# Kernel tuning notes

Hardware: AMD Instinct MI355X
Metric: run time of the kernel (lower is better)

## Reference

```python
import jax, jax.numpy as jnp
import numpy as np

B = 65536
DIM = 8
HIS_LEN = 5
KIND_LEN = 10
HIS_ITEM_DIM = (1 + KIND_LEN) * DIM  # 88
ALL_DIM = DIM * (5 + KIND_LEN) + HIS_ITEM_DIM  # 208


def _linear_params(key, in_dim, out_dim):
    k1, k2 = jax.random.split(key)
    bound = 1.0 / np.sqrt(in_dim)
    w = jax.random.uniform(k1, (out_dim, in_dim), jnp.float32, -bound, bound)
    b = jax.random.uniform(k2, (out_dim,), jnp.float32, -bound, bound)
    return w, b


def setup_inputs() -> dict:
    key = jax.random.key(0)
    ks = jax.random.split(key, 20)
    inp = {
        'userid': jax.random.randint(ks[0], (B, 1), 0, 1000000),
        'itemid': jax.random.randint(ks[1], (B, 1), 0, 1000000),
        'user_age': jax.random.randint(ks[2], (B, 1), 0, 8),
        'gender': jax.random.randint(ks[3], (B, 1), 0, 3),
        'user_occupation': jax.random.randint(ks[4], (B, 1), 0, 25),
        'item_kind': jax.random.randint(ks[5], (B, KIND_LEN), 0, 20),
        'item_id_his': jax.random.randint(ks[6], (B, HIS_LEN), 0, 1000000),
        'item_kind_his': jax.random.randint(ks[7], (B, HIS_LEN, KIND_LEN), 0, 20),
        'user_emb': jax.random.normal(ks[8], (1000000, DIM), jnp.float32),
        'item_emb': jax.random.normal(ks[9], (1000000, DIM), jnp.float32),
        'age_emb': jax.random.normal(ks[10], (8, DIM), jnp.float32),
        'gender_emb': jax.random.normal(ks[11], (3, DIM), jnp.float32),
        'occ_emb': jax.random.normal(ks[12], (25, DIM), jnp.float32),
        'kind_emb': jax.random.normal(ks[13], (20, DIM), jnp.float32),
    }
    act_dims = [(HIS_ITEM_DIM * 3, 64), (64, 32), (32, 1)]
    for i, (di, do) in enumerate(act_dims, 1):
        w, b = _linear_params(jax.random.fold_in(key, 100 + i), di, do)
        inp[f'act_w{i}'], inp[f'act_b{i}'] = w, b
    mlp_dims = [(ALL_DIM, 128), (128, 64), (64, 32), (32, 1)]
    for i, (di, do) in enumerate(mlp_dims, 1):
        w, b = _linear_params(jax.random.fold_in(key, 200 + i), di, do)
        inp[f'mlp_w{i}'], inp[f'mlp_b{i}'] = w, b
    return inp


def _forward(userid, itemid, user_age, gender, user_occupation, item_kind,
             item_id_his, item_kind_his, user_emb, item_emb, age_emb,
             gender_emb, occ_emb, kind_emb,
             act_w1, act_b1, act_w2, act_b2, act_w3, act_b3,
             mlp_w1, mlp_b1, mlp_w2, mlp_b2, mlp_w3, mlp_b3, mlp_w4, mlp_b4):
    b = userid.shape[0]
    user_w = user_emb[userid]          # [b,1,8]
    item_w = item_emb[itemid]          # [b,1,8]
    age_w = age_emb[user_age]          # [b,1,8]
    gen_w = gender_emb[gender]         # [b,1,8]
    occ_w = occ_emb[user_occupation]   # [b,1,8]
    kind_w = kind_emb[item_kind]       # [b,10,8]
    kind_w = kind_w * (item_kind != 0)[..., None].astype(kind_w.dtype)

    # history: vectorized over his_len
    his_item_w = item_emb[item_id_his]           # [b,5,8]
    his_kind_w = kind_emb[item_kind_his]         # [b,5,10,8]
    his_kind_w = his_kind_w * (item_kind_his != 0)[..., None].astype(his_kind_w.dtype)
    his_feature = jnp.concatenate([his_item_w[:, :, None, :], his_kind_w], axis=2)
    his_feature = his_feature.reshape(b, HIS_LEN, HIS_ITEM_DIM)  # [b,5,88]

    item_feat_now = jnp.concatenate([item_w, kind_w], axis=1).reshape(b, 1, HIS_ITEM_DIM)
    item_feat_now = jnp.broadcast_to(item_feat_now, (b, HIS_LEN, HIS_ITEM_DIM))

    # ActUnit: i_in = [i1, i1-i2, i2]; score = MLP(i_in); act_weight = i1 * score
    i1, i2 = his_feature, item_feat_now
    i_in = jnp.concatenate([i1, i1 - i2, i2], axis=-1)  # [b,5,264]
    h = jax.nn.relu(jnp.einsum('bsd,od->bso', i_in, act_w1) + act_b1)
    h = jax.nn.relu(jnp.einsum('bsd,od->bso', h, act_w2) + act_b2)
    score = jnp.einsum('bsd,od->bso', h, act_w3) + act_b3  # [b,5,1]
    act_weight = i1 * score
    his_pool = jnp.sum(his_feature * act_weight, axis=1)  # [b,88]

    all_feat = jnp.concatenate([user_w, item_w, age_w, gen_w, occ_w, kind_w], axis=1).reshape(b, -1)
    all_feat = jnp.concatenate([all_feat, his_pool], axis=-1)  # [b,208]

    h = jax.nn.relu(all_feat @ mlp_w1.T + mlp_b1)
    h = jax.nn.relu(h @ mlp_w2.T + mlp_b2)
    h = jax.nn.relu(h @ mlp_w3.T + mlp_b3)
    logit = h @ mlp_w4.T + mlp_b4  # [b,1]
    return jax.nn.sigmoid(logit)


def reference(userid, itemid, user_age, gender, user_occupation, item_kind,
              item_id_his, item_kind_his, user_emb, item_emb, age_emb,
              gender_emb, occ_emb, kind_emb,
              act_w1, act_b1, act_w2, act_b2, act_w3, act_b3,
              mlp_w1, mlp_b1, mlp_w2, mlp_b2, mlp_w3, mlp_b3, mlp_w4, mlp_b4):
    return _forward(userid, itemid, user_age, gender, user_occupation, item_kind,
                    item_id_his, item_kind_his, user_emb, item_emb, age_emb,
                    gender_emb, occ_emb, kind_emb,
                    act_w1, act_b1, act_w2, act_b2, act_w3, act_b3,
                    mlp_w1, mlp_b1, mlp_w2, mlp_b2, mlp_w3, mlp_b3, mlp_w4, mlp_b4)
```

## Files before the change

kernel.cpp:

```cpp
#include <hip/hip_runtime.h>
#include <cstdint>
#include <math.h>

#define BATCH    65536
#define HIS_LEN  5
#define KIND_LEN 10
#define SB       64
#define NTH      256

typedef float    v2f __attribute__((ext_vector_type(2)));
typedef float    v4f __attribute__((ext_vector_type(4)));
typedef _Float16 v2h __attribute__((ext_vector_type(2)));
typedef _Float16 v8h __attribute__((ext_vector_type(8)));
__device__ __forceinline__ v2f mk2(float a, float b){ v2f r; r.x=a; r.y=b; return r; }
#define C2H(u)  __builtin_bit_cast(v2h,(unsigned)(u))
#define C8H(u4) __builtin_bit_cast(v8h,(u4))

#if __has_builtin(__builtin_amdgcn_fdot2)
__device__ __forceinline__ float FD2(v2h a, v2h b, float c){
  return __builtin_amdgcn_fdot2(a, b, c, false);
}
#else
__device__ __forceinline__ float FD2(v2h a, v2h b, float c){
  return c + (float)a.x*(float)b.x + (float)a.y*(float)b.y;
}
#endif

__device__ __forceinline__ unsigned short f2h(float f){
  return __builtin_bit_cast(unsigned short, (_Float16)f);
}
__device__ __forceinline__ unsigned pack2h(float a, float b){
  return (unsigned)f2h(a) | ((unsigned)f2h(b) << 16);
}
__device__ __forceinline__ v2h pkh(float a, float b){
  return __builtin_bit_cast(v2h, __builtin_amdgcn_cvt_pkrtz(a, b));
}

#define OFF_HW1F 0
#define OFF_AW2F 6144
#define OFF_PF   7168
#define OFF_M3H  7428
#define OFF_MW1F 8452
#define OFF_MB1  22788
#define OFF_MW2F 22916
#define PREP_N   27012
#define AW2F4 1536
#define M3H4  1857
#define MW1F4 2113
#define MW2F4 5729

#define X2B   0
#define X1B   832
#define H1B   1664
#define H2B   2240
#define M3HL  2816
#define LAB1  12312
#define LAB2  12376
#define LW3   12408
#define LAB3  12440
#define LMB2  12441
#define LMB3  12505
#define LM4   12537
#define LMB4  12569
#define MB1F  12572
#define LDSF  12700

typedef const float* fp;

__device__ __forceinline__ float m1s_val(fp m1, int o, int q, int t){
  if(t >= 52) return 0.f;
  int src;
  if(t<8){ int E = (q==0)?0:(8+8*q); src = E + t; }
  else if(t<30){ int d=t-8; int idx = 8*(d>>1)+2*q+(d&1);
                 src = (idx<8) ? (8+idx) : (32+idx); }
  else { int d=t-30; int idx = 8*(d>>1)+2*q+(d&1); src = 120+idx; }
  return m1[o*208 + src];
}
__device__ __forceinline__ float m1k(fp m1, int o, int k){
  return m1s_val(m1, o, k/56, k%56);
}
__device__ __forceinline__ float w1c_val(fp aw1, int o, int q, int h, int d){
  if(d >= 22) return 0.f;
  int idx = 8*(d>>1) + 2*q + (d&1);
  return h ? (aw1[o*264+176+idx] - aw1[o*264+88+idx])
           : (aw1[o*264+idx]     + aw1[o*264+88+idx]);
}
__device__ __forceinline__ float hw1v(fp aw1, int o, int k){
  int h = (k >= 96) ? 1 : 0;
  int kk = k - 96*h;
  int q = kk/24, d = kk%24;
  return (d<22) ? w1c_val(aw1,o,q,h,d) : 0.f;
}

__global__ void din_prep(fp aw1, fp ab1, fp aw2, fp ab2, fp aw3, fp ab3,
                         fp m1,  fp mb1, fp m2,  fp mb2, fp m3,  fp mb3,
                         fp m4,  fp mb4, float* __restrict__ ws){
  int j = blockIdx.x*blockDim.x + threadIdx.x;
  unsigned* wsu = (unsigned*)ws;
  if(j < 6144){
    int frag = j>>2, jr = j&3;
    int lane = frag & 63, nt = frag >> 6;
    int n = nt/6, t = nt%6;
    int o = 16*n + (lane&15);
    int k0 = t*32 + ((lane>>4)<<3) + 2*jr;
    wsu[OFF_HW1F + j] = pack2h(hw1v(aw1,o,k0), hw1v(aw1,o,k0+1));
    return;
  } j -= 6144;
  if(j < 1024){
    int frag = j>>2, jr = j&3;
    int lane = frag & 63, nt = frag >> 6;
    int n2 = nt>>1, t2 = nt&1;
    int o = 16*n2 + (lane&15);
    int k0 = t2*32 + ((lane>>4)<<3) + 2*jr;
    wsu[OFF_AW2F + j] = pack2h(aw2[o*64 + k0], aw2[o*64 + k0+1]);
    return;
  } j -= 1024;
  if(j < 258){
    float v;
    if(j < 64)       v = ab1[j];
    else if(j < 96)  v = ab2[j-64];
    else if(j < 128) v = aw3[j-96];
    else if(j < 129) v = ab3[0];
    else if(j < 193) v = mb2[j-129];
    else if(j < 225) v = mb3[j-193];
    else if(j < 257) v = m4[j-225];
    else             v = mb4[0];
    ws[OFF_PF + j] = v; return;
  } j -= 258;
  if(j < 2){ ws[OFF_PF+258+j] = 0.f; return; } j -= 2;
  if(j < 1024){
    int qq = j>>8, rr = j&255, ip = rr>>5, dw = rr&31;
    wsu[OFF_M3H + j] = pack2h(m3[dw*64 + 16*qq + 2*ip], m3[dw*64 + 16*qq + 2*ip+1]);
    return;
  } j -= 1024;
  if(j < 14336){
    int frag = j>>2, jr = j&3;
    int lane = frag & 63, nt = frag >> 6;
    int n = nt/7, t = nt - 7*n;
    int o = 16*n + (lane&15);
    int k0 = t*32 + ((lane>>4)<<3) + 2*jr;
    wsu[OFF_MW1F + j] = pack2h(m1k(m1,o,k0), m1k(m1,o,k0+1));
    return;
  } j -= 14336;
  if(j < 128){ ws[OFF_MB1 + j] = mb1[j]; return; } j -= 128;
  if(j < 4096){
    int frag = j>>2, jr = j&3;
    int lane = frag & 63, nt = frag >> 6;
    int n2 = nt>>2, t2 = nt&3;
    int o = 16*n2 + (lane&15);
    int k0 = t2*32 + ((lane>>4)<<3) + 2*jr;
    wsu[OFF_MW2F + j] = pack2h(m2[o*128 + k0], m2[o*128 + k0+1]);
    return;
  }
}

template<int CTL>
__device__ __forceinline__ float qp(float v){
  return __uint_as_float((unsigned)__builtin_amdgcn_update_dpp(
      0, (int)__float_as_uint(v), CTL, 0xF, 0xF, true));
}
__device__ __forceinline__ float bsum4(float v){
  v += qp<0xB1>(v);
  v += qp<0x4E>(v);
  return v;
}

__device__ __forceinline__ void ldst16(void* l, const void* g){
  __builtin_amdgcn_global_load_lds(
      (const __attribute__((address_space(1))) unsigned int*)(uintptr_t)g,
      (__attribute__((address_space(3))) unsigned int*)(uintptr_t)l, 16, 0, 0);
}
__device__ __forceinline__ void ldst4(void* l, const void* g){
  __builtin_amdgcn_global_load_lds(
      (const __attribute__((address_space(1))) unsigned int*)(uintptr_t)g,
      (__attribute__((address_space(3))) unsigned int*)(uintptr_t)l, 4, 0, 0);
}

__device__ __forceinline__ void gather_h(const float2* __restrict__ itemp,
                                         const float2* __restrict__ kindp,
                                         int item_idx, const int* __restrict__ kidx,
                                         int q, v2h* f){
  float2 v = itemp[item_idx*4 + q];
  f[0] = pkh(v.x, v.y);
  #pragma unroll
  for(int r=0;r<KIND_LEN;r++){
    int ki = kidx[r];
    float2 w = kindp[ki*4 + q];
    float mx = ki ? w.x : 0.f, my = ki ? w.y : 0.f;
    f[1+r] = pkh(mx, my);
  }
}

__device__ __forceinline__ void write_X(float4* ls4, int base, int wid, int q,
                                        const v2h* f){
  unsigned xd[12];
  #pragma unroll
  for(int r=0;r<11;r++) xd[r] = __builtin_bit_cast(unsigned, f[r]);
  xd[11] = 0;
  uint4* xp = (uint4*)(ls4 + base + wid*13 + 3*q);
  #pragma unroll
  for(int c=0;c<3;c++){
    uint4 t; t.x=xd[4*c]; t.y=xd[4*c+1]; t.z=xd[4*c+2]; t.w=xd[4*c+3];
    xp[c] = t;
  }
}

__global__ void __launch_bounds__(NTH, 3)
din_main(const int* __restrict__ userid, const int* __restrict__ itemid,
         const int* __restrict__ age,    const int* __restrict__ gen,
         const int* __restrict__ occ,    const int* __restrict__ item_kind,
         const int* __restrict__ his_id, const int* __restrict__ his_kind,
         const float2* __restrict__ user_emb, const float2* __restrict__ item_emb,
         const float2* __restrict__ age_emb,  const float2* __restrict__ gen_emb,
         const float2* __restrict__ occ_emb,  const float2* __restrict__ kind_emb,
         const float* __restrict__ ws, float* __restrict__ out){
  const int tid  = threadIdx.x;
  const int q    = tid & 3;
  const int sl   = (tid & 63) >> 2;
  const int wv   = __builtin_amdgcn_readfirstlane(tid >> 6);
  const int wid  = wv*16 + sl;
  const int b    = blockIdx.x*SB + wid;
  const int l    = tid & 63;
  const int sr   = wv*16 + (l&15);
  const int kb   = l >> 4;

  __shared__ __align__(16) float ls[LDSF];
  float4* ls4 = (float4*)ls;
  const uint4* lsu4 = (const uint4*)ls;
  const float* wsc = ws;
  const float4* ws4 = (const float4*)ws;
  const uint4* wsu4 = (const uint4*)ws;

  ldst4(ls + LAB1 + tid, wsc + OFF_PF + tid);
  if(tid < 2)   ldst4(ls + LAB1 + 256 + tid, wsc + OFF_PF + 256 + tid);
  if(tid < 128) ldst4(ls + MB1F + tid, wsc + OFF_MB1 + tid);
  ldst16(ls4 + M3HL + (tid>>6)*66 + (tid&63), ws4 + M3H4 + tid);

  {
    v2h i2t[11];
    gather_h(item_emb, kind_emb, itemid[b], item_kind + b*KIND_LEN, q, i2t);
    write_X(ls4, X2B, wid, q, i2t);
  }
  v2h i1c[11], i1n[11];
  gather_h(item_emb, kind_emb, his_id[b*HIS_LEN], his_kind + b*HIS_LEN*KIND_LEN,
           q, i1c);

  v2f poolv[11];
  #pragma unroll
  for(int d=0;d<11;d++) poolv[d]=mk2(0.f,0.f);
  v2h i2h[11];
  float2 exr[4];

  __syncthreads();

  #pragma unroll 1
  for(int s=0;s<5;s++){
    write_X(ls4, X1B, wid, q, i1c);
    __syncthreads();
    if(s < 4){
      gather_h(item_emb, kind_emb, his_id[b*HIS_LEN+s+1],
               his_kind + (b*HIS_LEN+s+1)*KIND_LEN, q, i1n);
    } else {
      gather_h(item_emb, kind_emb, itemid[b], item_kind + b*KIND_LEN, q, i2h);
      const float2* ep = (q==0)? user_emb : (q==1)? age_emb : (q==2)? gen_emb : occ_emb;
      int ei = (q==0)? userid[b] : (q==1)? age[b] : (q==2)? gen[b] : occ[b];
      #pragma unroll
      for(int k=0;k<4;k++) exr[k] = ep[ei*4+k];
    }
    {
      uint4 a1[6];
      #pragma unroll
      for(int t=0;t<3;t++) a1[t]   = lsu4[X2B*0 + X1B + sr*13 + 4*t + kb];
      #pragma unroll
      for(int t=0;t<3;t++) a1[3+t] = lsu4[X2B + sr*13 + 4*t + kb];
      _Float16* h1p = (_Float16*)(ls4 + H1B);
      #pragma unroll
      for(int n=0;n<4;n++){
        float bb = ls[LAB1 + 16*n + (l&15)];
        v4f c = {bb,bb,bb,bb};
        #pragma unroll
        for(int t=0;t<6;t++){
          uint4 bw = wsu4[(n*6+t)*64 + l];
          c = __builtin_amdgcn_mfma_f32_16x16x32_f16(C8H(a1[t]), C8H(bw), c, 0, 0, 0);
        }
        #pragma unroll
        for(int i=0;i<4;i++)
          h1p[(16*wv + 4*kb + i)*72 + 16*n + (l&15)] = (_Float16)fmaxf(c[i],0.f);
      }
    }
    __syncthreads();
    {
      uint4 a2[2];
      #pragma unroll
      for(int t=0;t<2;t++) a2[t] = lsu4[H1B + sr*9 + 4*t + kb];
      float* h2p = (float*)(ls4 + H2B);
      #pragma unroll
      for(int n2=0;n2<2;n2++){
        float bb = ls[LAB2 + 16*n2 + (l&15)];
        v4f c = {bb,bb,bb,bb};
        #pragma unroll
        for(int t=0;t<2;t++){
          uint4 bw = wsu4[AW2F4 + (n2*2+t)*64 + l];
          c = __builtin_amdgcn_mfma_f32_16x16x32_f16(C8H(a2[t]), C8H(bw), c, 0, 0, 0);
        }
        #pragma unroll
        for(int i=0;i<4;i++)
          h2p[(16*wv + 4*kb + i)*36 + 16*n2 + (l&15)] = fmaxf(c[i],0.f);
      }
    }
    __syncthreads();
    {
      const float4* hr = (const float4*)(ls4 + H2B + wid*9 + 2*q);
      float4 h0 = hr[0], h1v = hr[1];
      float scp = h0.x*ls[LW3+8*q]   + h0.y*ls[LW3+8*q+1]
                + h0.z*ls[LW3+8*q+2] + h0.w*ls[LW3+8*q+3]
                + h1v.x*ls[LW3+8*q+4] + h1v.y*ls[LW3+8*q+5]
                + h1v.z*ls[LW3+8*q+6] + h1v.w*ls[LW3+8*q+7];
      float sc = bsum4(scp) + ls[LAB3];
      #pragma unroll
      for(int j=0;j<11;j++){
        float sx = (float)i1c[j].x, sy = (float)i1c[j].y;
        poolv[j] = __builtin_elementwise_fma(mk2(sx*sc, sy*sc), mk2(sx, sy), poolv[j]);
      }
    }
    #pragma unroll
    for(int j=0;j<11;j++) i1c[j] = i1n[j];
  }

  v2h fe[26];
  #pragma unroll
  for(int k=0;k<4;k++) fe[k] = pkh(exr[k].x, exr[k].y);
  #pragma unroll
  for(int j=0;j<11;j++) fe[4+j]  = i2h[j];
  #pragma unroll
  for(int j=0;j<11;j++) fe[15+j] = pkh(poolv[j].x, poolv[j].y);

  {
    unsigned xd[28];
    #pragma unroll
    for(int u=0;u<26;u++) xd[u] = __builtin_bit_cast(unsigned, fe[u]);
    xd[26] = 0; xd[27] = 0;
    uint4* xp = (uint4*)(ls4 + wid*29 + q*7);
    #pragma unroll
    for(int ct=0; ct<7; ct++){
      uint4 t; t.x=xd[4*ct]; t.y=xd[4*ct+1]; t.z=xd[4*ct+2]; t.w=xd[4*ct+3];
      xp[ct] = t;
    }
  }
  __syncthreads();

  uint4 af[7];
  #pragma unroll
  for(int t=0;t<7;t++) af[t] = lsu4[sr*29 + t*4 + kb];
  __syncthreads();

  v4f acc1[8];
  #pragma unroll
  for(int n=0;n<8;n++){
    float bb = ls[MB1F + n*16 + (l&15)];
    v4f c = {bb, bb, bb, bb};
    #pragma unroll
    for(int t=0;t<7;t++){
      uint4 bw = wsu4[MW1F4 + (n*7+t)*64 + l];
      c = __builtin_amdgcn_mfma_f32_16x16x32_f16(C8H(af[t]), C8H(bw), c, 0, 0, 0);
    }
    acc1[n] = c;
  }
  {
    _Float16* h1p = (_Float16*)ls;
    #pragma unroll
    for(int n=0;n<8;n++)
      #pragma unroll
      for(int i=0;i<4;i++)
        h1p[(16*wv + 4*kb + i)*136 + 16*n + (l&15)] =
            (_Float16)fmaxf(acc1[n][i], 0.f);
  }
  __syncthreads();

  v4f acc2[4];
  #pragma unroll
  for(int n2=0;n2<4;n2++){
    float bb = ls[LMB2 + n2*16 + (l&15)];
    v4f c = {bb, bb, bb, bb};
    acc2[n2] = c;
  }
  #pragma unroll
  for(int t2=0;t2<4;t2++){
    uint4 aw = lsu4[sr*17 + t2*4 + kb];
    #pragma unroll
    for(int n2=0;n2<4;n2++){
      uint4 bw = wsu4[MW2F4 + (n2*4+t2)*64 + l];
      acc2[n2] = __builtin_amdgcn_mfma_f32_16x16x32_f16(C8H(aw), C8H(bw), acc2[n2], 0, 0, 0);
    }
  }
  {
    _Float16* h2p = (_Float16*)(ls4 + 1088);
    #pragma unroll
    for(int n2=0;n2<4;n2++)
      #pragma unroll
      for(int i=0;i<4;i++)
        h2p[(16*wv + 4*kb + i)*72 + 16*n2 + (l&15)] =
            (_Float16)fmaxf(acc2[n2][i], 0.f);
  }
  __syncthreads();

  v2h hp3[8];
  {
    const uint4* hr = (const uint4*)(ls4 + 1088 + wid*9 + 2*q);
    uint4 d0 = hr[0], d1 = hr[1];
    hp3[0]=C2H(d0.x); hp3[1]=C2H(d0.y); hp3[2]=C2H(d0.z); hp3[3]=C2H(d0.w);
    hp3[4]=C2H(d1.x); hp3[5]=C2H(d1.y); hp3[6]=C2H(d1.z); hp3[7]=C2H(d1.w);
  }
  float x = ls[LMB4];
  #pragma unroll
  for(int g=0;g<4;g++){
    float a[8];
    #pragma unroll
    for(int j=0;j<8;j++) a[j]=0.f;
    #pragma unroll
    for(int ip=0;ip<8;ip++){
      const uint4* w3p = (const uint4*)(ls4 + M3HL + q*66 + ip*8 + 2*g);
      uint4 b0=w3p[0], b1=w3p[1];
      a[0]=FD2(C2H(b0.x),hp3[ip],a[0]); a[1]=FD2(C2H(b0.y),hp3[ip],a[1]);
      a[2]=FD2(C2H(b0.z),hp3[ip],a[2]); a[3]=FD2(C2H(b0.w),hp3[ip],a[3]);
      a[4]=FD2(C2H(b1.x),hp3[ip],a[4]); a[5]=FD2(C2H(b1.y),hp3[ip],a[5]);
      a[6]=FD2(C2H(b1.z),hp3[ip],a[6]); a[7]=FD2(C2H(b1.w),hp3[ip],a[7]);
    }
    #pragma unroll
    for(int j=0;j<8;j++) a[j] = bsum4(a[j]);
    #pragma unroll
    for(int j=0;j<8;j++)
      x += ls[LM4+8*g+j] * fmaxf(a[j] + ls[LMB3+8*g+j], 0.f);
  }

  if(q==0) out[b] = 1.0f/(1.0f + __expf(-x));
}

extern "C" void kernel_launch(void* const* d_in, const int* in_sizes, int n_in,
                              void* d_out, int out_size, void* d_ws, size_t ws_size,
                              hipStream_t stream){
  const int* userid    = (const int*)d_in[0];
  const int* itemid    = (const int*)d_in[1];
  const int* age       = (const int*)d_in[2];
  const int* gen       = (const int*)d_in[3];
  const int* occ       = (const int*)d_in[4];
  const int* item_kind = (const int*)d_in[5];
  const int* his_id    = (const int*)d_in[6];
  const int* his_kind  = (const int*)d_in[7];
  const float2* user_emb = (const float2*)d_in[8];
  const float2* item_emb = (const float2*)d_in[9];
  const float2* age_emb  = (const float2*)d_in[10];
  const float2* gen_emb  = (const float2*)d_in[11];
  const float2* occ_emb  = (const float2*)d_in[12];
  const float2* kind_emb = (const float2*)d_in[13];
  float* ws = (float*)d_ws;

  din_prep<<<(PREP_N+255)/256, 256, 0, stream>>>(
      (fp)d_in[14], (fp)d_in[15], (fp)d_in[16], (fp)d_in[17], (fp)d_in[18], (fp)d_in[19],
      (fp)d_in[20], (fp)d_in[21], (fp)d_in[22], (fp)d_in[23], (fp)d_in[24], (fp)d_in[25],
      (fp)d_in[26], (fp)d_in[27], ws);

  din_main<<<BATCH/SB, NTH, 0, stream>>>(
      userid, itemid, age, gen, occ, item_kind, his_id, his_kind,
      user_emb, item_emb, age_emb, gen_emb, occ_emb, kind_emb,
      ws, (float*)d_out);
}
```

Measured before the change: 238.1 us.

## Replace block barriers with wave-local LDS waits and hoist loop-invariant loads

Swaps most __syncthreads calls in the history-attention loop and the final MLP for an s_waitcnt lgkmcnt(0) plus a scheduling barrier. This relies on each wave only reading LDS rows it wrote itself. It also hoists the bias, the layer-3 weights and the act layer-2 weight fragments into registers before the loop, so they are not reloaded on every iteration. This removes block-wide barrier stalls and repeated LDS reads, at the cost of more registers and a correctness risk if any cross-wave LDS dependency still exists.

```diff
diff --git a/kernel.cpp b/kernel.cpp
--- a/kernel.cpp
+++ b/kernel.cpp
@@ -34,6 +34,11 @@
 }
 __device__ __forceinline__ v2h pkh(float a, float b){
   return __builtin_bit_cast(v2h, __builtin_amdgcn_cvt_pkrtz(a, b));
+}
+
+__device__ __forceinline__ void wlf(){
+  asm volatile("s_waitcnt lgkmcnt(0)" ::: "memory");
+  __builtin_amdgcn_sched_barrier(0);
 }
 
 #define OFF_HW1F 0
@@ -253,10 +258,22 @@
 
   __syncthreads();
 
+  float hb1[4], hb2[2], w3r[8];
+  #pragma unroll
+  for(int n=0;n<4;n++)  hb1[n] = ls[LAB1 + 16*n + (l&15)];
+  #pragma unroll
+  for(int n2=0;n2<2;n2++) hb2[n2] = ls[LAB2 + 16*n2 + (l&15)];
+  #pragma unroll
+  for(int k=0;k<8;k++)  w3r[k] = ls[LW3 + 8*q + k];
+  const float ab3v = ls[LAB3];
+  uint4 awf[4];
+  #pragma unroll
+  for(int t=0;t<4;t++) awf[t] = wsu4[AW2F4 + t*64 + l];
+
   #pragma unroll 1
   for(int s=0;s<5;s++){
+    wlf();
     write_X(ls4, X1B, wid, q, i1c);
-    __syncthreads();
     if(s < 4){
       gather_h(item_emb, kind_emb, his_id[b*HIS_LEN+s+1],
                his_kind + (b*HIS_LEN+s+1)*KIND_LEN, q, i1n);
@@ -267,16 +284,17 @@
       #pragma unroll
       for(int k=0;k<4;k++) exr[k] = ep[ei*4+k];
     }
+    wlf();
     {
       uint4 a1[6];
       #pragma unroll
-      for(int t=0;t<3;t++) a1[t]   = lsu4[X2B*0 + X1B + sr*13 + 4*t + kb];
+      for(int t=0;t<3;t++) a1[t]   = lsu4[X1B + sr*13 + 4*t + kb];
       #pragma unroll
       for(int t=0;t<3;t++) a1[3+t] = lsu4[X2B + sr*13 + 4*t + kb];
       _Float16* h1p = (_Float16*)(ls4 + H1B);
       #pragma unroll
       for(int n=0;n<4;n++){
-        float bb = ls[LAB1 + 16*n + (l&15)];
+        float bb = hb1[n];
         v4f c = {bb,bb,bb,bb};
         #pragma unroll
         for(int t=0;t<6;t++){
@@ -288,7 +306,7 @@
           h1p[(16*wv + 4*kb + i)*72 + 16*n + (l&15)] = (_Float16)fmaxf(c[i],0.f);
       }
     }
-    __syncthreads();
+    wlf();
     {
       uint4 a2[2];
       #pragma unroll
@@ -296,11 +314,11 @@
       float* h2p = (float*)(ls4 + H2B);
       #pragma unroll
       for(int n2=0;n2<2;n2++){
-        float bb = ls[LAB2 + 16*n2 + (l&15)];
+        float bb = hb2[n2];
         v4f c = {bb,bb,bb,bb};
         #pragma unroll
         for(int t=0;t<2;t++){
-          uint4 bw = wsu4[AW2F4 + (n2*2+t)*64 + l];
+          uint4 bw = awf[n2*2+t];
           c = __builtin_amdgcn_mfma_f32_16x16x32_f16(C8H(a2[t]), C8H(bw), c, 0, 0, 0);
         }
         #pragma unroll
@@ -308,15 +326,13 @@
           h2p[(16*wv + 4*kb + i)*36 + 16*n2 + (l&15)] = fmaxf(c[i],0.f);
       }
     }
-    __syncthreads();
+    wlf();
     {
       const float4* hr = (const float4*)(ls4 + H2B + wid*9 + 2*q);
       float4 h0 = hr[0], h1v = hr[1];
-      float scp = h0.x*ls[LW3+8*q]   + h0.y*ls[LW3+8*q+1]
-                + h0.z*ls[LW3+8*q+2] + h0.w*ls[LW3+8*q+3]
-                + h1v.x*ls[LW3+8*q+4] + h1v.y*ls[LW3+8*q+5]
-                + h1v.z*ls[LW3+8*q+6] + h1v.w*ls[LW3+8*q+7];
-      float sc = bsum4(scp) + ls[LAB3];
+      float scp = h0.x*w3r[0] + h0.y*w3r[1] + h0.z*w3r[2] + h0.w*w3r[3]
+                + h1v.x*w3r[4] + h1v.y*w3r[5] + h1v.z*w3r[6] + h1v.w*w3r[7];
+      float sc = bsum4(scp) + ab3v;
       #pragma unroll
       for(int j=0;j<11;j++){
         float sx = (float)i1c[j].x, sy = (float)i1c[j].y;
@@ -335,6 +351,8 @@
   #pragma unroll
   for(int j=0;j<11;j++) fe[15+j] = pkh(poolv[j].x, poolv[j].y);
 
+  __syncthreads();
+
   {
     unsigned xd[28];
     #pragma unroll
@@ -347,8 +365,7 @@
       xp[ct] = t;
     }
   }
-  __syncthreads();
-
+  wlf();
   uint4 af[7];
   #pragma unroll
   for(int t=0;t<7;t++) af[t] = lsu4[sr*29 + t*4 + kb];
@@ -375,7 +392,7 @@
         h1p[(16*wv + 4*kb + i)*136 + 16*n + (l&15)] =
             (_Float16)fmaxf(acc1[n][i], 0.f);
   }
-  __syncthreads();
+  wlf();
 
   v4f acc2[4];
   #pragma unroll
@@ -402,7 +419,7 @@
         h2p[(16*wv + 4*kb + i)*72 + 16*n2 + (l&15)] =
             (_Float16)fmaxf(acc2[n2][i], 0.f);
   }
-  __syncthreads();
+  wlf();
 
   v2h hp3[8];
   {
```

New measurement: 284.9 us. 1.2x slower.

## Fuse attention score layer into registers and shrink LDS for higher occupancy

Applied to the files above, without the earlier changes.

The attention MLP's second-layer outputs are no longer stored to LDS and reloaded for the final dot product. The score is now computed directly from the MFMA accumulators with 16-lane cross-lane reductions, which also removes one barrier per history step. Layer biases and final-layer weights are hoisted into registers before the loop. The H2 buffer is gone and the MLP-3 weight prefetch now reuses the freed region after the feature read, so the LDS footprint shrinks and launch bounds rise to 4 blocks per CU. The cost is the reordered prefetch and overlapping LDS regions, which depend on correct barrier placement.

```diff
diff --git a/kernel.cpp b/kernel.cpp
--- a/kernel.cpp
+++ b/kernel.cpp
@@ -52,18 +52,17 @@
 #define X2B   0
 #define X1B   832
 #define H1B   1664
-#define H2B   2240
-#define M3HL  2816
-#define LAB1  12312
-#define LAB2  12376
-#define LW3   12408
-#define LAB3  12440
-#define LMB2  12441
-#define LMB3  12505
-#define LM4   12537
-#define LMB4  12569
-#define MB1F  12572
-#define LDSF  12700
+#define M3HL  1664
+#define LAB1  8960
+#define LAB2  9024
+#define LW3   9056
+#define LAB3  9088
+#define LMB2  9089
+#define LMB3  9153
+#define LM4   9185
+#define LMB4  9217
+#define MB1F  9220
+#define LDSF  9348
 
 typedef const float* fp;
 
@@ -164,6 +163,13 @@
   v += qp<0x4E>(v);
   return v;
 }
+__device__ __forceinline__ float rsum16(float v){
+  v += qp<0xB1>(v);
+  v += qp<0x4E>(v);
+  v += __shfl_xor(v, 4);
+  v += __shfl_xor(v, 8);
+  return v;
+}
 
 __device__ __forceinline__ void ldst16(void* l, const void* g){
   __builtin_amdgcn_global_load_lds(
@@ -205,7 +211,7 @@
   }
 }
 
-__global__ void __launch_bounds__(NTH, 3)
+__global__ void __launch_bounds__(NTH, 4)
 din_main(const int* __restrict__ userid, const int* __restrict__ itemid,
          const int* __restrict__ age,    const int* __restrict__ gen,
          const int* __restrict__ occ,    const int* __restrict__ item_kind,
@@ -234,7 +240,6 @@
   ldst4(ls + LAB1 + tid, wsc + OFF_PF + tid);
   if(tid < 2)   ldst4(ls + LAB1 + 256 + tid, wsc + OFF_PF + 256 + tid);
   if(tid < 128) ldst4(ls + MB1F + tid, wsc + OFF_MB1 + tid);
-  ldst16(ls4 + M3HL + (tid>>6)*66 + (tid&63), ws4 + M3H4 + tid);
 
   {
     v2h i2t[11];
@@ -252,6 +257,16 @@
   float2 exr[4];
 
   __syncthreads();
+
+  float hb1[4], hb2[2];
+  #pragma unroll
+  for(int n=0;n<4;n++)  hb1[n] = ls[LAB1 + 16*n + (l&15)];
+  #pragma unroll
+  for(int n2=0;n2<2;n2++) hb2[n2] = ls[LAB2 + 16*n2 + (l&15)];
+  const float w3a = ls[LW3 + (l&15)];
+  const float w3b = ls[LW3 + 16 + (l&15)];
+  const float ab3v = ls[LAB3];
+  const int ii = (l>>2)&3;
 
   #pragma unroll 1
   for(int s=0;s<5;s++){
@@ -270,13 +285,13 @@
     {
       uint4 a1[6];
       #pragma unroll
-      for(int t=0;t<3;t++) a1[t]   = lsu4[X2B*0 + X1B + sr*13 + 4*t + kb];
+      for(int t=0;t<3;t++) a1[t]   = lsu4[X1B + sr*13 + 4*t + kb];
       #pragma unroll
       for(int t=0;t<3;t++) a1[3+t] = lsu4[X2B + sr*13 + 4*t + kb];
       _Float16* h1p = (_Float16*)(ls4 + H1B);
       #pragma unroll
       for(int n=0;n<4;n++){
-        float bb = ls[LAB1 + 16*n + (l&15)];
+        float bb = hb1[n];
         v4f c = {bb,bb,bb,bb};
         #pragma unroll
         for(int t=0;t<6;t++){
@@ -289,34 +304,29 @@
       }
     }
     __syncthreads();
+    v4f c20, c21;
     {
       uint4 a2[2];
       #pragma unroll
       for(int t=0;t<2;t++) a2[t] = lsu4[H1B + sr*9 + 4*t + kb];
-      float* h2p = (float*)(ls4 + H2B);
-      #pragma unroll
-      for(int n2=0;n2<2;n2++){
-        float bb = ls[LAB2 + 16*n2 + (l&15)];
-        v4f c = {bb,bb,bb,bb};
-        #pragma unroll
-        for(int t=0;t<2;t++){
-          uint4 bw = wsu4[AW2F4 + (n2*2+t)*64 + l];
-          c = __builtin_amdgcn_mfma_f32_16x16x32_f16(C8H(a2[t]), C8H(bw), c, 0, 0, 0);
-        }
-        #pragma unroll
-        for(int i=0;i<4;i++)
-          h2p[(16*wv + 4*kb + i)*36 + 16*n2 + (l&15)] = fmaxf(c[i],0.f);
+      c20 = (v4f){hb2[0],hb2[0],hb2[0],hb2[0]};
+      c21 = (v4f){hb2[1],hb2[1],hb2[1],hb2[1]};
+      #pragma unroll
+      for(int t=0;t<2;t++){
+        uint4 bw0 = wsu4[AW2F4 + t*64 + l];
+        uint4 bw1 = wsu4[AW2F4 + (2+t)*64 + l];
+        c20 = __builtin_amdgcn_mfma_f32_16x16x32_f16(C8H(a2[t]), C8H(bw0), c20, 0, 0, 0);
+        c21 = __builtin_amdgcn_mfma_f32_16x16x32_f16(C8H(a2[t]), C8H(bw1), c21, 0, 0, 0);
       }
     }
-    __syncthreads();
     {
-      const float4* hr = (const float4*)(ls4 + H2B + wid*9 + 2*q);
-      float4 h0 = hr[0], h1v = hr[1];
-      float scp = h0.x*ls[LW3+8*q]   + h0.y*ls[LW3+8*q+1]
-                + h0.z*ls[LW3+8*q+2] + h0.w*ls[LW3+8*q+3]
-                + h1v.x*ls[LW3+8*q+4] + h1v.y*ls[LW3+8*q+5]
-                + h1v.z*ls[LW3+8*q+6] + h1v.w*ls[LW3+8*q+7];
-      float sc = bsum4(scp) + ls[LAB3];
+      float p0 = w3a*fmaxf(c20[0],0.f) + w3b*fmaxf(c21[0],0.f);
+      float p1 = w3a*fmaxf(c20[1],0.f) + w3b*fmaxf(c21[1],0.f);
+      float p2 = w3a*fmaxf(c20[2],0.f) + w3b*fmaxf(c21[2],0.f);
+      float p3 = w3a*fmaxf(c20[3],0.f) + w3b*fmaxf(c21[3],0.f);
+      p0 = rsum16(p0); p1 = rsum16(p1); p2 = rsum16(p2); p3 = rsum16(p3);
+      float scp = (ii==0)? p0 : (ii==1)? p1 : (ii==2)? p2 : p3;
+      float sc = scp + ab3v;
       #pragma unroll
       for(int j=0;j<11;j++){
         float sx = (float)i1c[j].x, sy = (float)i1c[j].y;
@@ -335,6 +345,8 @@
   #pragma unroll
   for(int j=0;j<11;j++) fe[15+j] = pkh(poolv[j].x, poolv[j].y);
 
+  __syncthreads();
+
   {
     unsigned xd[28];
     #pragma unroll
@@ -348,11 +360,12 @@
     }
   }
   __syncthreads();
-
   uint4 af[7];
   #pragma unroll
   for(int t=0;t<7;t++) af[t] = lsu4[sr*29 + t*4 + kb];
   __syncthreads();
+
+  ldst16(ls4 + M3HL + (tid>>6)*66 + (tid&63), ws4 + M3H4 + tid);
 
   v4f acc1[8];
   #pragma unroll
```

After: 271.7 us. +14.1%, slower.
